# Optimization experiments

Hardware: AMD Instinct MI355X
Metric: run time of the kernel (lower is better)

The kernel has to match this reference:

```python
import jax, jax.numpy as jnp
import numpy as np

HIDDEN = 128
GLOBAL_HIDDEN = 128
STATE_DIM = 8
FEATURE = HIDDEN + GLOBAL_HIDDEN + STATE_DIM  # 264, as in SympleAgent.feature_size
NUM_OPS = 30
NUM_INTERNAL_OPS = 5
N_NODES = 400000


def _ffn(x, W1, b1, W2, b2):
    # FFN(in, hidden, out, n_layers=1): Linear -> ReLU -> Linear
    return jax.nn.relu(x @ W1 + b1) @ W2 + b2


def setup_inputs() -> dict:
    key = jax.random.key(0)
    ks = jax.random.split(key, 20)
    s = 0.02

    def lin(k, fan_in, fan_out):
        k1, k2 = jax.random.split(k)
        return (jax.random.normal(k1, (fan_in, fan_out), jnp.float32) * s,
                jax.random.normal(k2, (fan_out,), jnp.float32) * s)

    W_hl1, b_hl1 = lin(ks[0], FEATURE, HIDDEN)
    W_hl2, b_hl2 = lin(ks[1], HIDDEN, 4)            # high_level_actor -> 4
    W_in1, b_in1 = lin(ks[2], FEATURE, HIDDEN)
    W_in2, b_in2 = lin(ks[3], HIDDEN, NUM_INTERNAL_OPS)  # internal_actor
    W_ex1, b_ex1 = lin(ks[4], FEATURE, HIDDEN)
    W_ex2, b_ex2 = lin(ks[5], HIDDEN, NUM_OPS)      # actor (external ops)
    W_tp1, b_tp1 = lin(ks[6], FEATURE, HIDDEN)
    W_tp2, b_tp2 = lin(ks[7], HIDDEN, 1)            # teleport_ffn -> 1 per node

    node_hidden = jax.random.normal(ks[8], (N_NODES, HIDDEN), jnp.float32)
    h_glob = jax.random.normal(ks[9], (1, GLOBAL_HIDDEN), jnp.float32)
    state_tensor = jax.random.normal(ks[10], (1, STATE_DIM), jnp.float32)
    validity_mask = jnp.ones((1, NUM_OPS), jnp.float32)

    return {
        "node_hidden": node_hidden, "h_glob": h_glob,
        "state_tensor": state_tensor, "validity_mask": validity_mask,
        "W_hl1": W_hl1, "b_hl1": b_hl1, "W_hl2": W_hl2, "b_hl2": b_hl2,
        "W_in1": W_in1, "b_in1": b_in1, "W_in2": W_in2, "b_in2": b_in2,
        "W_ex1": W_ex1, "b_ex1": b_ex1, "W_ex2": W_ex2, "b_ex2": b_ex2,
        "W_tp1": W_tp1, "b_tp1": b_tp1, "W_tp2": W_tp2, "b_tp2": b_tp2,
    }


def reference(node_hidden, h_glob, state_tensor, validity_mask,
              W_hl1, b_hl1, W_hl2, b_hl2,
              W_in1, b_in1, W_in2, b_in2,
              W_ex1, b_ex1, W_ex2, b_ex2,
              W_tp1, b_tp1, W_tp2, b_tp2):
    # --- get_policy_logits for current node (coord -> node 0) ---
    cur = node_hidden[0:1]                                   # [1, H]
    feats = jnp.concatenate([cur, h_glob, state_tensor], -1)  # [1, FEATURE]
    l_high = _ffn(feats, W_hl1, b_hl1, W_hl2, b_hl2)          # [1, 4]
    l_internal = _ffn(feats, W_in1, b_in1, W_in2, b_in2)      # [1, 5]
    l_ext = _ffn(feats, W_ex1, b_ex1, W_ex2, b_ex2) + jnp.log(validity_mask)  # [1, NUM_OPS]

    # --- apply_teleport_ffn: features over all n_nodes ---
    n = node_hidden.shape[0]
    hg = jnp.broadcast_to(h_glob, (n, h_glob.shape[-1]))      # h_glob[-1].repeat(n,1)
    st = jnp.broadcast_to(state_tensor, (n, state_tensor.shape[-1]))
    tp_feats = jnp.concatenate([hg, node_hidden, st], -1)     # [n, FEATURE]
    l_teleport = _ffn(tp_feats, W_tp1, b_tp1, W_tp2, b_tp2).T  # [1, n]

    # concatenate all heads along the logit axis: [1, 4 + 5 + NUM_OPS + n]
    return jnp.concatenate([l_high, l_internal, l_ext, l_teleport], axis=-1)
```

## Files before the change

### kernel.cpp

```cpp
#include <hip/hip_runtime.h>
#include <hip/hip_bf16.h>
#include <stdint.h>

typedef __attribute__((ext_vector_type(8))) short short8;
typedef __bf16 bf16x8 __attribute__((ext_vector_type(8)));
typedef __attribute__((ext_vector_type(4))) float f32x4;

#define HID 128
#define NTILES 8
#define KSTEPS 4

#define WS_C_F    8192
#define WS_W2_F   8320
#define WS_B2_F   8448

#define TP_BLOCKS   256
#define TP_WAVES    8
#define TP_THREADS  (TP_WAVES * 64)
#define TOTAL_TP_WAVES (TP_BLOCKS * TP_WAVES)

#define SLOT_BYTES    8192
#define AFRAG_BYTES   32768
#define SMEM_BYTES    (AFRAG_BYTES + TP_WAVES * 2 * SLOT_BYTES)

__global__ void prep_kernel(const float* __restrict__ node_hidden,
                            const float* __restrict__ h_glob,
                            const float* __restrict__ state,
                            const float* __restrict__ validity,
                            const float* __restrict__ W_hl1, const float* __restrict__ b_hl1,
                            const float* __restrict__ W_hl2, const float* __restrict__ b_hl2,
                            const float* __restrict__ W_in1, const float* __restrict__ b_in1,
                            const float* __restrict__ W_in2, const float* __restrict__ b_in2,
                            const float* __restrict__ W_ex1, const float* __restrict__ b_ex1,
                            const float* __restrict__ W_ex2, const float* __restrict__ b_ex2,
                            const float* __restrict__ W_tp1, const float* __restrict__ b_tp1,
                            const float* __restrict__ W_tp2, const float* __restrict__ b_tp2,
                            float* __restrict__ out, float* __restrict__ ws)
{
    const int tid = threadIdx.x;
    const int b = blockIdx.x;

    if (b < 3) {
        __shared__ float feats[264];
        __shared__ float hpart[4][128];
        __shared__ float hidden[128];
        const float* W1 = (b == 0) ? W_hl1 : (b == 1 ? W_in1 : W_ex1);
        const float* b1 = (b == 0) ? b_hl1 : (b == 1 ? b_in1 : b_ex1);
        const float* W2 = (b == 0) ? W_hl2 : (b == 1 ? W_in2 : W_ex2);
        const float* b2 = (b == 0) ? b_hl2 : (b == 1 ? b_in2 : b_ex2);
        const int od    = (b == 0) ? 4 : (b == 1 ? 5 : 30);
        const int obase = (b == 0) ? 0 : (b == 1 ? 4 : 9);

        if (tid < 264) {
            float v;
            if (tid < 128)      v = node_hidden[tid];
            else if (tid < 256) v = h_glob[tid - 128];
            else                v = state[tid - 256];
            feats[tid] = v;
        }
        __syncthreads();
        {
            const int j = tid & 127, q = tid >> 7;
            float s = 0.f;
            for (int i = q * 66; i < q * 66 + 66; ++i) s += feats[i] * W1[i * 128 + j];
            hpart[q][j] = s;
        }
        __syncthreads();
        if (tid < 128) {
            float h = b1[tid] + hpart[0][tid] + hpart[1][tid] + hpart[2][tid] + hpart[3][tid];
            hidden[tid] = fmaxf(h, 0.f);
        }
        __syncthreads();
        if (tid < od) {
            float o = b2[tid];
            for (int i = 0; i < 128; ++i) o += hidden[i] * W2[i * od + tid];
            if (b == 2) o += logf(validity[tid]);
            out[obase + tid] = o;
        }
    } else if (b == 3) {
        __shared__ float cpart[4][128];
        {
            const int j = tid & 127, q = tid >> 7;
            float s = 0.f;
            for (int i = q * 32; i < q * 32 + 32; ++i) s += h_glob[i] * W_tp1[i * HID + j];
            if (q == 3)
                for (int i = 0; i < 8; ++i) s += state[i] * W_tp1[(256 + i) * HID + j];
            cpart[q][j] = s;
        }
        __syncthreads();
        if (tid < 128) {
            ws[WS_C_F  + tid] = b_tp1[tid] + cpart[0][tid] + cpart[1][tid]
                                           + cpart[2][tid] + cpart[3][tid];
            ws[WS_W2_F + tid] = W_tp2[tid];
            if (tid == 0) ws[WS_B2_F] = b_tp2[0];
        }
    } else {
        short* afrag = (short*)ws;
        const int part = b - 4;
        for (int idx = part * 1024 + tid; idx < part * 1024 + 1024; idx += 512) {
            const int k = idx >> 7, nn = idx & 127;
            const int t = nn >> 4, cc = nn & 15;
            const int s = k >> 5, rr = k & 31;
            const int g = rr >> 3, j = rr & 7;
            const int lane = cc + (g << 4);
            afrag[(((t * KSTEPS + s) * 64 + lane) << 3) + j] =
                (short)__builtin_bit_cast(unsigned short, (__bf16)W_tp1[(128 + k) * HID + nn]);
        }
    }
}

__launch_bounds__(TP_THREADS)
__global__ void teleport_kernel(const float* __restrict__ node_hidden,
                                const float* __restrict__ ws,
                                float* __restrict__ out,
                                int n)
{
    __shared__ __align__(16) unsigned char smem[SMEM_BYTES];
    const int tid = threadIdx.x;

    const int lane = tid & 63;
    const int wave = tid >> 6;
    const int m  = lane & 15;
    const int g  = lane >> 4;
    const unsigned mx = (unsigned)(m & 7);
    const unsigned mrow = (unsigned)m * 512;

    {
        const int4* wsv = (const int4*)ws;
        int4* sv = (int4*)smem;
        for (int i = tid; i < 2048; i += TP_THREADS) sv[i] = wsv[i];
    }
    f32x4 cR[NTILES], wR[NTILES];
    #pragma unroll
    for (int t = 0; t < NTILES; ++t) {
        cR[t] = *(const f32x4*)(ws + WS_C_F  + t * 16 + g * 4);
        wR[t] = *(const f32x4*)(ws + WS_W2_F + t * 16 + g * 4);
    }
    const float bias2 = ws[WS_B2_F];
    __syncthreads();

    const short* afrag = (const short*)smem;

    unsigned char* p0 = smem + AFRAG_BYTES + wave * 2 * SLOT_BYTES;
    unsigned char* p1 = p0 + SLOT_BYTES;

    const int nChunks = (n + 15) >> 4;
    const int gw = blockIdx.x * TP_WAVES + wave;
    const int c0 = (int)(((long long)gw * nChunks) / TOTAL_TP_WAVES);
    const int c1 = (int)(((long long)(gw + 1) * nChunks) / TOTAL_TP_WAVES);

#define STAGE(slot_, c_)                                                         \
    {                                                                            \
        _Pragma("unroll")                                                        \
        for (int k_ = 0; k_ < 8; ++k_) {                                         \
            const int row_ = 2 * k_ + (lane >> 5);                               \
            const int grow_ = min((c_) * 16 + row_, n - 1);                      \
            const unsigned su_ = ((unsigned)(lane & 31)) ^ ((unsigned)(row_ & 7));\
            const unsigned char* src_ = (const unsigned char*)node_hidden        \
                                        + (size_t)grow_ * 512 + (su_ << 4);      \
            __builtin_amdgcn_global_load_lds(                                    \
                (const __attribute__((address_space(1))) unsigned int*)src_,     \
                (__attribute__((address_space(3))) unsigned int*)(slot_ + k_ * 1024), \
                16, 0, 0);                                                       \
        }                                                                        \
    }

    if (c0 < c1) {
        STAGE(p0, c0);
        if (c0 + 1 < c1) STAGE(p1, c0 + 1);

        for (int c = c0; c < c1; ++c) {
            if (c == c1 - 1)      { asm volatile("s_waitcnt vmcnt(0)"  ::: "memory"); }
            else if (c == c0)     { asm volatile("s_waitcnt vmcnt(8)"  ::: "memory"); }
            else if (c == c0 + 1) { asm volatile("s_waitcnt vmcnt(9)"  ::: "memory"); }
            else                  { asm volatile("s_waitcnt vmcnt(10)" ::: "memory"); }

            bf16x8 nd[KSTEPS];
            #pragma unroll
            for (int s = 0; s < KSTEPS; ++s) {
                const unsigned u0 = (((unsigned)(s * 8 + g * 2))     ^ mx) << 4;
                const unsigned u1 = (((unsigned)(s * 8 + g * 2 + 1)) ^ mx) << 4;
                const float4 fa = *(const float4*)(p0 + mrow + u0);
                const float4 fb = *(const float4*)(p0 + mrow + u1);
                bf16x8 a;
                a[0] = (__bf16)fa.x; a[1] = (__bf16)fa.y; a[2] = (__bf16)fa.z; a[3] = (__bf16)fa.w;
                a[4] = (__bf16)fb.x; a[5] = (__bf16)fb.y; a[6] = (__bf16)fb.z; a[7] = (__bf16)fb.w;
                nd[s] = a;
            }
            __builtin_amdgcn_sched_barrier(0);
            if (c + 2 < c1) STAGE(p0, c + 2);

            float sr = 0.f;
            #pragma unroll
            for (int t = 0; t < NTILES; ++t) {
                f32x4 acc = (f32x4){0.f, 0.f, 0.f, 0.f};
                #pragma unroll
                for (int s = 0; s < KSTEPS; ++s) {
                    const short8 wv = *(const short8*)&afrag[(((t * KSTEPS + s) * 64 + lane) << 3)];
                    const bf16x8 wf = __builtin_bit_cast(bf16x8, wv);
                    acc = __builtin_amdgcn_mfma_f32_16x16x32_bf16(wf, nd[s], acc, 0, 0, 0);
                }
                float h0 = acc[0] + cR[t][0], h1 = acc[1] + cR[t][1];
                float h2 = acc[2] + cR[t][2], h3 = acc[3] + cR[t][3];
                h0 = h0 > 0.f ? h0 : 0.f;  h1 = h1 > 0.f ? h1 : 0.f;
                h2 = h2 > 0.f ? h2 : 0.f;  h3 = h3 > 0.f ? h3 : 0.f;
                sr += h0 * wR[t][0] + h1 * wR[t][1] + h2 * wR[t][2] + h3 * wR[t][3];
            }

            sr += __shfl_xor(sr, 16, 64);
            sr += __shfl_xor(sr, 32, 64);

            if (lane < 16) {
                const int o = c * 16 + lane;
                if (o < n) out[o] = sr + bias2;
            }

            unsigned char* tmp = p0; p0 = p1; p1 = tmp;
        }
    }
#undef STAGE
}

extern "C" void kernel_launch(void* const* d_in, const int* in_sizes, int n_in,
                              void* d_out, int out_size, void* d_ws, size_t ws_size,
                              hipStream_t stream) {
    const float* node_hidden = (const float*)d_in[0];
    const float* h_glob      = (const float*)d_in[1];
    const float* state       = (const float*)d_in[2];
    const float* validity    = (const float*)d_in[3];
    const float* W_hl1 = (const float*)d_in[4];  const float* b_hl1 = (const float*)d_in[5];
    const float* W_hl2 = (const float*)d_in[6];  const float* b_hl2 = (const float*)d_in[7];
    const float* W_in1 = (const float*)d_in[8];  const float* b_in1 = (const float*)d_in[9];
    const float* W_in2 = (const float*)d_in[10]; const float* b_in2 = (const float*)d_in[11];
    const float* W_ex1 = (const float*)d_in[12]; const float* b_ex1 = (const float*)d_in[13];
    const float* W_ex2 = (const float*)d_in[14]; const float* b_ex2 = (const float*)d_in[15];
    const float* W_tp1 = (const float*)d_in[16]; const float* b_tp1 = (const float*)d_in[17];
    const float* W_tp2 = (const float*)d_in[18]; const float* b_tp2 = (const float*)d_in[19];

    float* out = (float*)d_out;
    float* ws  = (float*)d_ws;
    const int n = in_sizes[0] / HID;

    prep_kernel<<<20, 512, 0, stream>>>(node_hidden, h_glob, state, validity,
                                        W_hl1, b_hl1, W_hl2, b_hl2,
                                        W_in1, b_in1, W_in2, b_in2,
                                        W_ex1, b_ex1, W_ex2, b_ex2,
                                        W_tp1, b_tp1, W_tp2, b_tp2,
                                        out, ws);
    teleport_kernel<<<TP_BLOCKS, TP_THREADS, 0, stream>>>(node_hidden, ws, out + 39, n);
}
```

Baseline: 48.50 us.

## Move policy-head FFNs into teleport kernel and rebalance chunk split

Result: faster. 45.21 us (-6.8%).

```diff
diff --git a/kernel.cpp b/kernel.cpp
--- a/kernel.cpp
+++ b/kernel.cpp
@@ -19,65 +19,25 @@
 #define TP_THREADS  (TP_WAVES * 64)
 #define TOTAL_TP_WAVES (TP_BLOCKS * TP_WAVES)
 
+#define HEAD_WAVES 24
+#define HW_U 3
+#define NW_U 12
+#define TOTAL_U (HEAD_WAVES * HW_U + (TOTAL_TP_WAVES - HEAD_WAVES) * NW_U)
+
 #define SLOT_BYTES    8192
 #define AFRAG_BYTES   32768
 #define SMEM_BYTES    (AFRAG_BYTES + TP_WAVES * 2 * SLOT_BYTES)
 
-__global__ void prep_kernel(const float* __restrict__ node_hidden,
-                            const float* __restrict__ h_glob,
+__global__ void prep_kernel(const float* __restrict__ h_glob,
                             const float* __restrict__ state,
-                            const float* __restrict__ validity,
-                            const float* __restrict__ W_hl1, const float* __restrict__ b_hl1,
-                            const float* __restrict__ W_hl2, const float* __restrict__ b_hl2,
-                            const float* __restrict__ W_in1, const float* __restrict__ b_in1,
-                            const float* __restrict__ W_in2, const float* __restrict__ b_in2,
-                            const float* __restrict__ W_ex1, const float* __restrict__ b_ex1,
-                            const float* __restrict__ W_ex2, const float* __restrict__ b_ex2,
                             const float* __restrict__ W_tp1, const float* __restrict__ b_tp1,
                             const float* __restrict__ W_tp2, const float* __restrict__ b_tp2,
-                            float* __restrict__ out, float* __restrict__ ws)
+                            float* __restrict__ ws)
 {
     const int tid = threadIdx.x;
     const int b = blockIdx.x;
 
-    if (b < 3) {
-        __shared__ float feats[264];
-        __shared__ float hpart[4][128];
-        __shared__ float hidden[128];
-        const float* W1 = (b == 0) ? W_hl1 : (b == 1 ? W_in1 : W_ex1);
-        const float* b1 = (b == 0) ? b_hl1 : (b == 1 ? b_in1 : b_ex1);
-        const float* W2 = (b == 0) ? W_hl2 : (b == 1 ? W_in2 : W_ex2);
-        const float* b2 = (b == 0) ? b_hl2 : (b == 1 ? b_in2 : b_ex2);
-        const int od    = (b == 0) ? 4 : (b == 1 ? 5 : 30);
-        const int obase = (b == 0) ? 0 : (b == 1 ? 4 : 9);
-
-        if (tid < 264) {
-            float v;
-            if (tid < 128)      v = node_hidden[tid];
-            else if (tid < 256) v = h_glob[tid - 128];
-            else                v = state[tid - 256];
-            feats[tid] = v;
-        }
-        __syncthreads();
-        {
-            const int j = tid & 127, q = tid >> 7;
-            float s = 0.f;
-            for (int i = q * 66; i < q * 66 + 66; ++i) s += feats[i] * W1[i * 128 + j];
-            hpart[q][j] = s;
-        }
-        __syncthreads();
-        if (tid < 128) {
-            float h = b1[tid] + hpart[0][tid] + hpart[1][tid] + hpart[2][tid] + hpart[3][tid];
-            hidden[tid] = fmaxf(h, 0.f);
-        }
-        __syncthreads();
-        if (tid < od) {
-            float o = b2[tid];
-            for (int i = 0; i < 128; ++i) o += hidden[i] * W2[i * od + tid];
-            if (b == 2) o += logf(validity[tid]);
-            out[obase + tid] = o;
-        }
-    } else if (b == 3) {
+    if (b == 0) {
         __shared__ float cpart[4][128];
         {
             const int j = tid & 127, q = tid >> 7;
@@ -96,7 +56,7 @@
         }
     } else {
         short* afrag = (short*)ws;
-        const int part = b - 4;
+        const int part = b - 1;
         for (int idx = part * 1024 + tid; idx < part * 1024 + 1024; idx += 512) {
             const int k = idx >> 7, nn = idx & 127;
             const int t = nn >> 4, cc = nn & 15;
@@ -111,6 +71,15 @@
 
 __launch_bounds__(TP_THREADS)
 __global__ void teleport_kernel(const float* __restrict__ node_hidden,
+                                const float* __restrict__ h_glob,
+                                const float* __restrict__ state,
+                                const float* __restrict__ validity,
+                                const float* __restrict__ W_hl1, const float* __restrict__ b_hl1,
+                                const float* __restrict__ W_hl2, const float* __restrict__ b_hl2,
+                                const float* __restrict__ W_in1, const float* __restrict__ b_in1,
+                                const float* __restrict__ W_in2, const float* __restrict__ b_in2,
+                                const float* __restrict__ W_ex1, const float* __restrict__ b_ex1,
+                                const float* __restrict__ W_ex2, const float* __restrict__ b_ex2,
                                 const float* __restrict__ ws,
                                 float* __restrict__ out,
                                 int n)
@@ -125,6 +94,47 @@
     const unsigned mx = (unsigned)(m & 7);
     const unsigned mrow = (unsigned)m * 512;
 
+    if (blockIdx.x < 3) {
+        float* feats  = (float*)(smem + AFRAG_BYTES);
+        float* hpart  = feats + 264;
+        float* hidden = hpart + 512;
+        const int b = blockIdx.x;
+        const float* W1 = (b == 0) ? W_hl1 : (b == 1 ? W_in1 : W_ex1);
+        const float* b1 = (b == 0) ? b_hl1 : (b == 1 ? b_in1 : b_ex1);
+        const float* W2 = (b == 0) ? W_hl2 : (b == 1 ? W_in2 : W_ex2);
+        const float* b2 = (b == 0) ? b_hl2 : (b == 1 ? b_in2 : b_ex2);
+        const int od    = (b == 0) ? 4 : (b == 1 ? 5 : 30);
+        const int obase = (b == 0) ? 0 : (b == 1 ? 4 : 9);
+
+        if (tid < 264) {
+            float v;
+            if (tid < 128)      v = node_hidden[tid];
+            else if (tid < 256) v = h_glob[tid - 128];
+            else                v = state[tid - 256];
+            feats[tid] = v;
+        }
+        __syncthreads();
+        {
+            const int j = tid & 127, q = tid >> 7;
+            float s = 0.f;
+            for (int i = q * 66; i < q * 66 + 66; ++i) s += feats[i] * W1[i * 128 + j];
+            hpart[q * 128 + j] = s;
+        }
+        __syncthreads();
+        if (tid < 128) {
+            float h = b1[tid] + hpart[tid] + hpart[128 + tid] + hpart[256 + tid] + hpart[384 + tid];
+            hidden[tid] = fmaxf(h, 0.f);
+        }
+        __syncthreads();
+        if (tid < od) {
+            float o = b2[tid];
+            for (int i = 0; i < 128; ++i) o += hidden[i] * W2[i * od + tid];
+            if (b == 2) o += logf(validity[tid]);
+            out[obase + tid] = o;
+        }
+        __syncthreads();
+    }
+
     {
         const int4* wsv = (const int4*)ws;
         int4* sv = (int4*)smem;
@@ -140,14 +150,21 @@
     __syncthreads();
 
     const short* afrag = (const short*)smem;
+    float* tout = out + 39;
 
     unsigned char* p0 = smem + AFRAG_BYTES + wave * 2 * SLOT_BYTES;
     unsigned char* p1 = p0 + SLOT_BYTES;
 
     const int nChunks = (n + 15) >> 4;
     const int gw = blockIdx.x * TP_WAVES + wave;
-    const int c0 = (int)(((long long)gw * nChunks) / TOTAL_TP_WAVES);
-    const int c1 = (int)(((long long)(gw + 1) * nChunks) / TOTAL_TP_WAVES);
+    const long long cumA = (gw < HEAD_WAVES)
+        ? (long long)gw * HW_U
+        : (long long)HEAD_WAVES * HW_U + (long long)(gw - HEAD_WAVES) * NW_U;
+    const long long cumB = (gw + 1 <= HEAD_WAVES)
+        ? (long long)(gw + 1) * HW_U
+        : (long long)HEAD_WAVES * HW_U + (long long)(gw + 1 - HEAD_WAVES) * NW_U;
+    const int c0 = (int)(cumA * nChunks / TOTAL_U);
+    const int c1 = (int)(cumB * nChunks / TOTAL_U);
 
 #define STAGE(slot_, c_)                                                         \
     {                                                                            \
@@ -212,7 +229,7 @@
 
             if (lane < 16) {
                 const int o = c * 16 + lane;
-                if (o < n) out[o] = sr + bias2;
+                if (o < n) tout[o] = sr + bias2;
             }
 
             unsigned char* tmp = p0; p0 = p1; p1 = tmp;
@@ -241,11 +258,10 @@
     float* ws  = (float*)d_ws;
     const int n = in_sizes[0] / HID;
 
-    prep_kernel<<<20, 512, 0, stream>>>(node_hidden, h_glob, state, validity,
-                                        W_hl1, b_hl1, W_hl2, b_hl2,
-                                        W_in1, b_in1, W_in2, b_in2,
-                                        W_ex1, b_ex1, W_ex2, b_ex2,
-                                        W_tp1, b_tp1, W_tp2, b_tp2,
-                                        out, ws);
-    teleport_kernel<<<TP_BLOCKS, TP_THREADS, 0, stream>>>(node_hidden, ws, out + 39, n);
+    prep_kernel<<<17, 512, 0, stream>>>(h_glob, state, W_tp1, b_tp1, W_tp2, b_tp2, ws);
+    teleport_kernel<<<TP_BLOCKS, TP_THREADS, 0, stream>>>(node_hidden, h_glob, state, validity,
+                                                          W_hl1, b_hl1, W_hl2, b_hl2,
+                                                          W_in1, b_in1, W_in2, b_in2,
+                                                          W_ex1, b_ex1, W_ex2, b_ex2,
+                                                          ws, out, n);
 }
```
